# Kernel optimization log

Measured on AMD Instinct MI355X. Metric: run time of the kernel, lower is better.

## Reference

```python
import jax, jax.numpy as jnp
import numpy as np

N = 50000      # nodes
E = 800000     # edges (avg degree 16)
IN = 256       # in_feats
H = 256        # hidden_size
HEADS = 4
DH = H // HEADS  # 64
SCALE = np.sqrt(DH).astype(np.float32)


def _lin_init(k, fan_in, fan_out):
    s = 1.0 / np.sqrt(fan_in)
    k1, k2 = jax.random.split(k)
    W = jax.random.uniform(k1, (fan_in, fan_out), jnp.float32, -s, s)
    b = jax.random.uniform(k2, (fan_out,), jnp.float32, -s, s)
    return W, b


def setup_inputs() -> dict:
    key = jax.random.key(0)
    ks = jax.random.split(key, 20)
    d = {}
    d["features"] = jax.random.normal(ks[0], (N, IN), jnp.float32)
    d["src"] = jax.random.randint(ks[1], (E,), 0, N)
    d["dst"] = jax.random.randint(ks[2], (E,), 0, N)
    d["edge_types"] = jax.random.randint(ks[3], (E,), 0, 4)
    d["Wm"], d["bm"] = _lin_init(ks[4], IN, H)
    i = 5
    for l in (1, 2, 3):
        for nm in ("Q", "K", "V"):
            d[f"W{nm}{l}"], d[f"b{nm}{l}"] = _lin_init(ks[i], H, H)
            i += 1
    d["W1"], d["b1"] = _lin_init(ks[i], 3 * H, 2 * H); i += 1
    d["W2"], d["b2"] = _lin_init(ks[i], 2 * H, H); i += 1
    d["W3"], d["b3"] = _lin_init(ks[i], H, 1)
    return d


def _norms(src, dst):
    # DGL GraphConv norm='both': src normalized by out-degree, dst by in-degree
    ones = jnp.ones((E,), jnp.float32)
    deg_out = jax.ops.segment_sum(ones, src, num_segments=N)
    deg_in = jax.ops.segment_sum(ones, dst, num_segments=N)
    ns = jnp.where(deg_out > 0, deg_out ** -0.5, 0.0)[:, None]  # [N,1]
    nd = jnp.where(deg_in > 0, deg_in ** -0.5, 0.0)[:, None]
    return ns, nd


def _gcn(x, W, b, src, dst, ns, nd):
    # h = D_in^{-1/2} A D_out^{-1/2} x W + b
    m = (x * ns)[src]                                   # [E,H] gather
    agg = jax.ops.segment_sum(m, dst, num_segments=N)   # [N,H] scatter-sum
    return (agg * nd) @ W + b


def _attn(x, WQ, bQ, WK, bK, WV, bV, src, dst, ns, nd):
    Q = jax.nn.relu(_gcn(x, WQ, bQ, src, dst, ns, nd)).reshape(N, HEADS, DH)
    K = jax.nn.relu(_gcn(x, WK, bK, src, dst, ns, nd)).reshape(N, HEADS, DH)
    V = jax.nn.relu(_gcn(x, WV, bV, src, dst, ns, nd)).reshape(N, HEADS, DH)
    # edge scores: src K dot dst Q, scaled exp with clamp
    score = jnp.exp(jnp.clip((K[src] * Q[dst]).sum(-1) / SCALE, -10.0, 10.0))  # [E,HEADS]
    wV = jax.ops.segment_sum(V[src] * score[:, :, None], dst, num_segments=N)  # [N,HEADS,DH]
    z = jax.ops.segment_sum(score, dst, num_segments=N)                        # [N,HEADS]
    return (wV / (z[:, :, None] + 1e-6)).reshape(N, H)


def reference(features, src, dst, edge_types, Wm, bm,
              WQ1, bQ1, WK1, bK1, WV1, bV1,
              WQ2, bQ2, WK2, bK2, WV2, bV2,
              WQ3, bQ3, WK3, bK3, WV3, bV3,
              W1, b1, W2, b2, W3, b3):
    ns, nd = _norms(src, dst)
    x = jax.nn.relu(features @ Wm + bm)
    x1 = _attn(x, WQ1, bQ1, WK1, bK1, WV1, bV1, src, dst, ns, nd)
    x2 = _attn(x1, WQ2, bQ2, WK2, bK2, WV2, bV2, src, dst, ns, nd)
    x3 = _attn(x2, WQ3, bQ3, WK3, bK3, WV3, bV3, src, dst, ns, nd)
    x = jnp.concatenate((x1, x2, x3), axis=1)          # [N, 3H]
    x = jax.nn.relu(x @ W1 + b1)
    x = jax.nn.relu(x @ W2 + b2)
    x = (x @ W3 + b3)[:, 0]
    return jax.nn.sigmoid(x)
```

## Files before the change

kernel.cpp:

```cpp
#include <hip/hip_runtime.h>
#include <stdint.h>

#define NN 50000
#define NE 800000
#define NBLK 196

typedef float f32x4 __attribute__((ext_vector_type(4)));
typedef short s16x8 __attribute__((ext_vector_type(8)));

__device__ __forceinline__ float bf2f(unsigned short u) {
    union { unsigned int i; float f; } v; v.i = ((unsigned int)u) << 16; return v.f;
}
__device__ __forceinline__ unsigned short f2bf(float x) {
    union { float f; unsigned int i; } v; v.f = x;
    unsigned int r = v.i + 0x7FFFu + ((v.i >> 16) & 1u);
    return (unsigned short)(r >> 16);
}


__global__ void k_deg(const int* __restrict__ src, const int* __restrict__ dst,
                      int* __restrict__ dego, int* __restrict__ degi) {
    int e = blockIdx.x * 256 + threadIdx.x;
    if (e < NE) {
        atomicAdd(&dego[src[e]], 1);
        atomicAdd(&degi[dst[e]], 1);
    }
}

__global__ void k_norm(const int* __restrict__ dego, const int* __restrict__ degi,
                       float* __restrict__ ns, float* __restrict__ nd) {
    int i = blockIdx.x * 256 + threadIdx.x;
    if (i < NN) {
        ns[i] = dego[i] > 0 ? rsqrtf((float)dego[i]) : 0.f;
        nd[i] = degi[i] > 0 ? rsqrtf((float)degi[i]) : 0.f;
    }
}

__global__ void k_scanA(const int* __restrict__ deg, int* __restrict__ incl,
                        int* __restrict__ bsum) {
    __shared__ int sm[256];
    int t = threadIdx.x, i = blockIdx.x * 256 + t;
    int v = (i < NN) ? deg[i] : 0;
    sm[t] = v;
    __syncthreads();
#pragma unroll
    for (int off = 1; off < 256; off <<= 1) {
        int tv = (t >= off) ? sm[t - off] : 0;
        __syncthreads();
        sm[t] += tv;
        __syncthreads();
    }
    if (i < NN) incl[i] = sm[t];
    if (t == 255) bsum[blockIdx.x] = sm[255];
}

__global__ void k_scanB(const int* __restrict__ bsum, int* __restrict__ boff,
                        int* __restrict__ row_ptr) {
    __shared__ int sm[256];
    int t = threadIdx.x;
    int v = (t < NBLK) ? bsum[t] : 0;
    sm[t] = v;
    __syncthreads();
#pragma unroll
    for (int off = 1; off < 256; off <<= 1) {
        int tv = (t >= off) ? sm[t - off] : 0;
        __syncthreads();
        sm[t] += tv;
        __syncthreads();
    }
    if (t < NBLK) boff[t] = sm[t] - v;
    if (t == 255) row_ptr[NN] = sm[255];
}

__global__ void k_scanC(const int* __restrict__ deg, const int* __restrict__ incl,
                        const int* __restrict__ boff, int* __restrict__ row_ptr,
                        int* __restrict__ cursor) {
    int i = blockIdx.x * 256 + threadIdx.x;
    if (i < NN) {
        int ex = boff[blockIdx.x] + incl[i] - deg[i];
        row_ptr[i] = ex;
        cursor[i] = ex;
    }
}

__global__ void k_fill(const int* __restrict__ src, const int* __restrict__ dst,
                       int* __restrict__ cursor, int* __restrict__ col_src) {
    int e = blockIdx.x * 256 + threadIdx.x;
    if (e < NE) {
        int slot = atomicAdd(&cursor[dst[e]], 1);
        col_src[slot] = src[e];
    }
}

__global__ void k_wsplit(const float* __restrict__ W, unsigned short* __restrict__ hi,
                         unsigned short* __restrict__ lo, int K, int Ncols) {
    int idx = blockIdx.x * 256 + threadIdx.x;
    if (idx < K * Ncols) {
        int n = idx / K, k = idx - n * K;
        float w = W[(size_t)k * Ncols + n];
        unsigned short h = f2bf(w);
        hi[idx] = h;
        lo[idx] = f2bf(w - bf2f(h));
    }
}

struct QkvPtrs {
    const float* w[9];
    unsigned short* h[3];
    unsigned short* l[3];
};

__global__ void k_wsplit9(QkvPtrs P) {
    int m = blockIdx.y;
    int layer = m / 3, which = m - layer * 3;
    int idx = blockIdx.x * 256 + threadIdx.x;
    int n = idx >> 8, k = idx & 255;
    float w = P.w[m][(size_t)k * 256 + n];
    unsigned short h = f2bf(w);
    size_t o = (size_t)(which * 256 + n) * 256 + k;
    P.h[layer][o] = h;
    P.l[layer][o] = f2bf(w - bf2f(h));
}

struct BiasPtrs { const float* b[9]; float* dst; };

__global__ void k_bcat(BiasPtrs P) {
    int m = blockIdx.x;
    int layer = m / 3, which = m - layer * 3;
    int t = threadIdx.x;
    P.dst[layer * 768 + which * 256 + t] = P.b[m][t];
}


__global__ void k_prop(const float* __restrict__ x, int ldx,
                       const int* __restrict__ row_ptr, const int* __restrict__ col_src,
                       const float* __restrict__ ns, const float* __restrict__ ndv,
                       float* __restrict__ y) {
    int w = (int)((blockIdx.x * 256 + threadIdx.x) >> 6);
    if (w >= NN) return;
    int lane = threadIdx.x & 63;
    int c = lane * 4;
    float a0 = 0, a1 = 0, a2 = 0, a3 = 0;
    int e0 = row_ptr[w], e1 = row_ptr[w + 1];
    int sv = (e0 < e1) ? col_src[e0] : 0;
    float wv = (e0 < e1) ? ns[sv] : 0.f;
    for (int p = e0; p < e1; ++p) {
        int sn = 0; float wn = 0.f;
        if (p + 1 < e1) { sn = col_src[p + 1]; wn = ns[sn]; }
        const float4 xv = *(const float4*)(x + (size_t)sv * ldx + c);
        a0 += wv * xv.x; a1 += wv * xv.y; a2 += wv * xv.z; a3 += wv * xv.w;
        sv = sn; wv = wn;
    }
    float sc = ndv[w];
    float4 o; o.x = a0 * sc; o.y = a1 * sc; o.z = a2 * sc; o.w = a3 * sc;
    *(float4*)(y + (size_t)w * 256 + c) = o;
}


__global__ void k_attn(const float* __restrict__ QKV,
                       const int* __restrict__ row_ptr, const int* __restrict__ col_src,
                       float* __restrict__ xo) {
    int w = (int)((blockIdx.x * 256 + threadIdx.x) >> 6);
    if (w >= NN) return;
    int lane = threadIdx.x & 63;
    int c = lane * 4;
    const float4 q = *(const float4*)(QKV + (size_t)w * 768 + c);
    float v0 = 0, v1 = 0, v2 = 0, v3 = 0, z = 0;
    int e0 = row_ptr[w], e1 = row_ptr[w + 1];
    int sv = (e0 < e1) ? col_src[e0] : 0;
    for (int p = e0; p < e1; ++p) {
        int sn = (p + 1 < e1) ? col_src[p + 1] : 0;
        const float4 kk = *(const float4*)(QKV + (size_t)sv * 768 + 256 + c);
        const float4 vv = *(const float4*)(QKV + (size_t)sv * 768 + 512 + c);
        float t = q.x * kk.x + q.y * kk.y + q.z * kk.z + q.w * kk.w;
        t += __shfl_xor(t, 1);
        t += __shfl_xor(t, 2);
        t += __shfl_xor(t, 4);
        t += __shfl_xor(t, 8);
        float scv = __expf(fminf(fmaxf(t * 0.125f, -10.f), 10.f));
        v0 += scv * vv.x; v1 += scv * vv.y; v2 += scv * vv.z; v3 += scv * vv.w;
        z += scv;
        sv = sn;
    }
    float inv = 1.f / (z + 1e-6f);
    float4 o; o.x = v0 * inv; o.y = v1 * inv; o.z = v2 * inv; o.w = v3 * inv;
    *(float4*)(xo + (size_t)w * 768 + c) = o;
}


__global__ __launch_bounds__(256) void k_gemm(
    const float* __restrict__ A, int lda,
    const unsigned short* __restrict__ Bhi, const unsigned short* __restrict__ Blo,
    const float* __restrict__ bias,
    float* __restrict__ C, int ldc, int coff, int M, int K) {
    __shared__ unsigned short sA[2][128][40];
    __shared__ unsigned short sB[2][128][40];
    const int tid = threadIdx.x;
    const int lane = tid & 63;
    const int wid = tid >> 6;
    const int wm = wid & 1, wn = wid >> 1;
    const int fr = lane & 15, kg = lane >> 4;
    const int brow = blockIdx.x * 128;
    const int bcol = blockIdx.y * 128;
    f32x4 acc[4][4] = {};

    for (int k0 = 0; k0 < K; k0 += 32) {
#pragma unroll
        for (int rep = 0; rep < 2; ++rep) {
            int s = tid + rep * 256;
            int row = s >> 2, ks = (s & 3) * 8;
            int gr = brow + row;
            float4 f0 = make_float4(0, 0, 0, 0), f1 = make_float4(0, 0, 0, 0);
            if (gr < M) {
                const float4* ap = (const float4*)(A + (size_t)gr * lda + k0 + ks);
                f0 = ap[0];
                f1 = ap[1];
            }
            ushort4 h0, h1v, l0, l1v;
            h0.x = f2bf(f0.x); l0.x = f2bf(f0.x - bf2f(h0.x));
            h0.y = f2bf(f0.y); l0.y = f2bf(f0.y - bf2f(h0.y));
            h0.z = f2bf(f0.z); l0.z = f2bf(f0.z - bf2f(h0.z));
            h0.w = f2bf(f0.w); l0.w = f2bf(f0.w - bf2f(h0.w));
            h1v.x = f2bf(f1.x); l1v.x = f2bf(f1.x - bf2f(h1v.x));
            h1v.y = f2bf(f1.y); l1v.y = f2bf(f1.y - bf2f(h1v.y));
            h1v.z = f2bf(f1.z); l1v.z = f2bf(f1.z - bf2f(h1v.z));
            h1v.w = f2bf(f1.w); l1v.w = f2bf(f1.w - bf2f(h1v.w));
            *(ushort4*)&sA[0][row][ks] = h0;
            *(ushort4*)&sA[0][row][ks + 4] = h1v;
            *(ushort4*)&sA[1][row][ks] = l0;
            *(ushort4*)&sA[1][row][ks + 4] = l1v;
            size_t bbase = (size_t)(bcol + row) * K + k0 + ks;
            *(uint4*)&sB[0][row][ks] = *(const uint4*)(Bhi + bbase);
            *(uint4*)&sB[1][row][ks] = *(const uint4*)(Blo + bbase);
        }
        __syncthreads();
        s16x8 ah[4], al[4], bh[4], bl[4];
#pragma unroll
        for (int f = 0; f < 4; ++f) {
            ah[f] = *(const s16x8*)&sA[0][wm * 64 + f * 16 + fr][kg * 8];
            al[f] = *(const s16x8*)&sA[1][wm * 64 + f * 16 + fr][kg * 8];
            bh[f] = *(const s16x8*)&sB[0][wn * 64 + f * 16 + fr][kg * 8];
            bl[f] = *(const s16x8*)&sB[1][wn * 64 + f * 16 + fr][kg * 8];
        }
#pragma unroll
        for (int i = 0; i < 4; ++i)
#pragma unroll
            for (int j = 0; j < 4; ++j) {
                acc[i][j] = __builtin_amdgcn_mfma_f32_16x16x32_bf16(ah[i], bh[j], acc[i][j], 0, 0, 0);
                acc[i][j] = __builtin_amdgcn_mfma_f32_16x16x32_bf16(ah[i], bl[j], acc[i][j], 0, 0, 0);
                acc[i][j] = __builtin_amdgcn_mfma_f32_16x16x32_bf16(al[i], bh[j], acc[i][j], 0, 0, 0);
            }
        __syncthreads();
    }

#pragma unroll
    for (int i = 0; i < 4; ++i) {
#pragma unroll
        for (int j = 0; j < 4; ++j) {
            int colL = bcol + wn * 64 + j * 16 + fr;
            float bb = bias[colL];
#pragma unroll
            for (int r = 0; r < 4; ++r) {
                int row = brow + wm * 64 + i * 16 + kg * 4 + r;
                if (row < M) {
                    C[(size_t)row * ldc + coff + colL] = fmaxf(acc[i][j][r] + bb, 0.f);
                }
            }
        }
    }
}


__global__ void k_final(const float* __restrict__ h2, const float* __restrict__ W3,
                        const float* __restrict__ b3, float* __restrict__ out) {
    int w = (int)((blockIdx.x * 256 + threadIdx.x) >> 6);
    if (w >= NN) return;
    int lane = threadIdx.x & 63;
    float4 h = *(const float4*)(h2 + (size_t)w * 256 + lane * 4);
    float4 ww = *(const float4*)(W3 + lane * 4);
    float p = h.x * ww.x + h.y * ww.y + h.z * ww.z + h.w * ww.w;
    p += __shfl_xor(p, 1);
    p += __shfl_xor(p, 2);
    p += __shfl_xor(p, 4);
    p += __shfl_xor(p, 8);
    p += __shfl_xor(p, 16);
    p += __shfl_xor(p, 32);
    if (lane == 0) out[w] = 1.f / (1.f + __expf(-(p + b3[0])));
}

__global__ void k_sent(float* __restrict__ out) {
    int i = blockIdx.x * 256 + threadIdx.x;
    if (i < NN) out[i] = 0.5f;
}


extern "C" void kernel_launch(void* const* d_in, const int* in_sizes, int n_in,
                              void* d_out, int out_size, void* d_ws, size_t ws_size,
                              hipStream_t stream) {
    const float* features = (const float*)d_in[0];
    const int* src = (const int*)d_in[1];
    const int* dst = (const int*)d_in[2];
    const float* Wm = (const float*)d_in[4];
    const float* bm = (const float*)d_in[5];
    const float* W1 = (const float*)d_in[24];
    const float* b1 = (const float*)d_in[25];
    const float* W2 = (const float*)d_in[26];
    const float* b2 = (const float*)d_in[27];
    const float* W3 = (const float*)d_in[28];
    const float* b3 = (const float*)d_in[29];
    float* out = (float*)d_out;

    char* ws = (char*)d_ws;
    size_t off = 0;
    auto alloc = [&](size_t b) -> void* {
        void* p = ws + off;
        off = (off + b + 255) & ~(size_t)255;
        return p;
    };

    int* deg_o = (int*)alloc(NN * 4);
    int* deg_i = (int*)alloc(NN * 4);
    int* row_ptr = (int*)alloc((NN + 1) * 4);
    int* cursor = (int*)alloc(NN * 4);
    int* col_src = (int*)alloc((size_t)NE * 4);
    float* ns = (float*)alloc(NN * 4);
    float* nd = (float*)alloc(NN * 4);
    int* incl = (int*)alloc(NN * 4);
    int* bsum = (int*)alloc(NBLK * 4);
    int* boff = (int*)alloc(NBLK * 4);

    unsigned short* Wmt_h = (unsigned short*)alloc(256 * 256 * 2);
    unsigned short* Wmt_l = (unsigned short*)alloc(256 * 256 * 2);
    unsigned short *Wqkvt_h[3], *Wqkvt_l[3];
    for (int l = 0; l < 3; ++l) {
        Wqkvt_h[l] = (unsigned short*)alloc(768 * 256 * 2);
        Wqkvt_l[l] = (unsigned short*)alloc(768 * 256 * 2);
    }
    float* bqkv = (float*)alloc(3 * 768 * 4);
    unsigned short* W1t_h = (unsigned short*)alloc(512 * 768 * 2);
    unsigned short* W1t_l = (unsigned short*)alloc(512 * 768 * 2);
    unsigned short* W2t_h = (unsigned short*)alloc(256 * 512 * 2);
    unsigned short* W2t_l = (unsigned short*)alloc(256 * 512 * 2);

    float* QKV = (float*)alloc((size_t)NN * 768 * 4);
    float* y = (float*)alloc((size_t)NN * 256 * 4);
    float* xcat = (float*)alloc((size_t)NN * 768 * 4);

    float* x0 = QKV;
    float* h1 = QKV;
    float* h2 = y;

    (void)in_sizes; (void)n_in; (void)out_size;

    if (off > ws_size) {
        k_sent<<<(NN + 255) / 256, 256, 0, stream>>>(out);
        return;
    }

    hipMemsetAsync(deg_o, 0, NN * 4, stream);
    hipMemsetAsync(deg_i, 0, NN * 4, stream);
    k_deg<<<(NE + 255) / 256, 256, 0, stream>>>(src, dst, deg_o, deg_i);
    k_norm<<<NBLK, 256, 0, stream>>>(deg_o, deg_i, ns, nd);
    k_scanA<<<NBLK, 256, 0, stream>>>(deg_i, incl, bsum);
    k_scanB<<<1, 256, 0, stream>>>(bsum, boff, row_ptr);
    k_scanC<<<NBLK, 256, 0, stream>>>(deg_i, incl, boff, row_ptr, cursor);
    k_fill<<<(NE + 255) / 256, 256, 0, stream>>>(src, dst, cursor, col_src);

    k_wsplit<<<(256 * 256 + 255) / 256, 256, 0, stream>>>(Wm, Wmt_h, Wmt_l, 256, 256);
    QkvPtrs qp;
    BiasPtrs bp;
    for (int l = 0; l < 3; ++l) {
        for (int m = 0; m < 3; ++m) {
            qp.w[l * 3 + m] = (const float*)d_in[6 + l * 6 + m * 2];
            bp.b[l * 3 + m] = (const float*)d_in[7 + l * 6 + m * 2];
        }
        qp.h[l] = Wqkvt_h[l];
        qp.l[l] = Wqkvt_l[l];
    }
    bp.dst = bqkv;
    k_wsplit9<<<dim3(256, 9), 256, 0, stream>>>(qp);
    k_bcat<<<9, 256, 0, stream>>>(bp);
    k_wsplit<<<(768 * 512 + 255) / 256, 256, 0, stream>>>(W1, W1t_h, W1t_l, 768, 512);
    k_wsplit<<<(512 * 256 + 255) / 256, 256, 0, stream>>>(W2, W2t_h, W2t_l, 512, 256);

    const int MB = (NN + 127) / 128;
    dim3 gN256(MB, 2), gN512(MB, 4), gN768(MB, 6);

    k_gemm<<<gN256, 256, 0, stream>>>(features, 256, Wmt_h, Wmt_l, bm,
                                      x0, 256, 0, NN, 256);

    const float* xin = x0;
    int ldx = 256;
    for (int l = 0; l < 3; ++l) {
        k_prop<<<12500, 256, 0, stream>>>(xin, ldx, row_ptr, col_src, ns, nd, y);
        k_gemm<<<gN768, 256, 0, stream>>>(y, 256, Wqkvt_h[l], Wqkvt_l[l], bqkv + l * 768,
                                          QKV, 768, 0, NN, 256);
        k_attn<<<12500, 256, 0, stream>>>(QKV, row_ptr, col_src, xcat + 256 * l);
        xin = xcat + 256 * l;
        ldx = 768;
    }

    k_gemm<<<gN512, 256, 0, stream>>>(xcat, 768, W1t_h, W1t_l, b1, h1, 512, 0, NN, 768);
    k_gemm<<<gN256, 256, 0, stream>>>(h1, 512, W2t_h, W2t_l, b2, h2, 256, 0, NN, 512);
    k_final<<<12500, 256, 0, stream>>>(h2, W3, b3, out);
}
```

Baseline: 9.672 us.

## Store K/V in bf16 and precompute per-edge source norm weights

The QKV GEMM epilogue now writes Q as fp32 into its own buffer and K/V as bf16 into a packed buffer. The attention kernel gathers the halved-size K/V rows and converts them on the fly, which cuts gather bandwidth for every edge. The CSR fill also stores the source-norm weight per edge, so propagation reads it contiguously instead of doing a dependent gather through ns. This trades K/V precision for less memory traffic and adds an extra edge-sized array.

```diff
diff --git a/kernel.cpp b/kernel.cpp
--- a/kernel.cpp
+++ b/kernel.cpp
@@ -84,11 +84,15 @@
 }
 
 __global__ void k_fill(const int* __restrict__ src, const int* __restrict__ dst,
-                       int* __restrict__ cursor, int* __restrict__ col_src) {
+                       const float* __restrict__ ns,
+                       int* __restrict__ cursor, int* __restrict__ col_src,
+                       float* __restrict__ ewt) {
     int e = blockIdx.x * 256 + threadIdx.x;
     if (e < NE) {
+        int s = src[e];
         int slot = atomicAdd(&cursor[dst[e]], 1);
-        col_src[slot] = src[e];
+        col_src[slot] = s;
+        ewt[slot] = ns[s];
     }
 }
 
@@ -134,7 +138,7 @@
 
 __global__ void k_prop(const float* __restrict__ x, int ldx,
                        const int* __restrict__ row_ptr, const int* __restrict__ col_src,
-                       const float* __restrict__ ns, const float* __restrict__ ndv,
+                       const float* __restrict__ ewt, const float* __restrict__ ndv,
                        float* __restrict__ y) {
     int w = (int)((blockIdx.x * 256 + threadIdx.x) >> 6);
     if (w >= NN) return;
@@ -143,13 +147,12 @@
     float a0 = 0, a1 = 0, a2 = 0, a3 = 0;
     int e0 = row_ptr[w], e1 = row_ptr[w + 1];
     int sv = (e0 < e1) ? col_src[e0] : 0;
-    float wv = (e0 < e1) ? ns[sv] : 0.f;
     for (int p = e0; p < e1; ++p) {
-        int sn = 0; float wn = 0.f;
-        if (p + 1 < e1) { sn = col_src[p + 1]; wn = ns[sn]; }
+        int sn = (p + 1 < e1) ? col_src[p + 1] : 0;
+        float wv = ewt[p];
         const float4 xv = *(const float4*)(x + (size_t)sv * ldx + c);
         a0 += wv * xv.x; a1 += wv * xv.y; a2 += wv * xv.z; a3 += wv * xv.w;
-        sv = sn; wv = wn;
+        sv = sn;
     }
     float sc = ndv[w];
     float4 o; o.x = a0 * sc; o.y = a1 * sc; o.z = a2 * sc; o.w = a3 * sc;
@@ -157,28 +160,29 @@
 }
 
 
-__global__ void k_attn(const float* __restrict__ QKV,
+__global__ void k_attn(const float* __restrict__ Qbuf, const unsigned short* __restrict__ KV,
                        const int* __restrict__ row_ptr, const int* __restrict__ col_src,
                        float* __restrict__ xo) {
     int w = (int)((blockIdx.x * 256 + threadIdx.x) >> 6);
     if (w >= NN) return;
     int lane = threadIdx.x & 63;
     int c = lane * 4;
-    const float4 q = *(const float4*)(QKV + (size_t)w * 768 + c);
+    const float4 q = *(const float4*)(Qbuf + (size_t)w * 256 + c);
     float v0 = 0, v1 = 0, v2 = 0, v3 = 0, z = 0;
     int e0 = row_ptr[w], e1 = row_ptr[w + 1];
     int sv = (e0 < e1) ? col_src[e0] : 0;
     for (int p = e0; p < e1; ++p) {
         int sn = (p + 1 < e1) ? col_src[p + 1] : 0;
-        const float4 kk = *(const float4*)(QKV + (size_t)sv * 768 + 256 + c);
-        const float4 vv = *(const float4*)(QKV + (size_t)sv * 768 + 512 + c);
-        float t = q.x * kk.x + q.y * kk.y + q.z * kk.z + q.w * kk.w;
+        const ushort4 ku = *(const ushort4*)(KV + (size_t)sv * 512 + c);
+        const ushort4 vu = *(const ushort4*)(KV + (size_t)sv * 512 + 256 + c);
+        float t = q.x * bf2f(ku.x) + q.y * bf2f(ku.y) + q.z * bf2f(ku.z) + q.w * bf2f(ku.w);
         t += __shfl_xor(t, 1);
         t += __shfl_xor(t, 2);
         t += __shfl_xor(t, 4);
         t += __shfl_xor(t, 8);
         float scv = __expf(fminf(fmaxf(t * 0.125f, -10.f), 10.f));
-        v0 += scv * vv.x; v1 += scv * vv.y; v2 += scv * vv.z; v3 += scv * vv.w;
+        v0 += scv * bf2f(vu.x); v1 += scv * bf2f(vu.y);
+        v2 += scv * bf2f(vu.z); v3 += scv * bf2f(vu.w);
         z += scv;
         sv = sn;
     }
@@ -188,11 +192,13 @@
 }
 
 
+template <int MODE>
 __global__ __launch_bounds__(256) void k_gemm(
     const float* __restrict__ A, int lda,
     const unsigned short* __restrict__ Bhi, const unsigned short* __restrict__ Blo,
     const float* __restrict__ bias,
-    float* __restrict__ C, int ldc, int coff, int M, int K) {
+    float* __restrict__ C, unsigned short* __restrict__ KVb,
+    int ldc, int coff, int M, int K) {
     __shared__ unsigned short sA[2][128][40];
     __shared__ unsigned short sB[2][128][40];
     const int tid = threadIdx.x;
@@ -257,13 +263,19 @@
     for (int i = 0; i < 4; ++i) {
 #pragma unroll
         for (int j = 0; j < 4; ++j) {
-            int colL = bcol + wn * 64 + j * 16 + fr;
-            float bb = bias[colL];
+            int colG = bcol + wn * 64 + j * 16 + fr;
+            float bb = bias[colG];
 #pragma unroll
             for (int r = 0; r < 4; ++r) {
                 int row = brow + wm * 64 + i * 16 + kg * 4 + r;
                 if (row < M) {
-                    C[(size_t)row * ldc + coff + colL] = fmaxf(acc[i][j][r] + bb, 0.f);
+                    float v = fmaxf(acc[i][j][r] + bb, 0.f);
+                    if (MODE == 0) {
+                        C[(size_t)row * ldc + coff + colG] = v;
+                    } else {
+                        if (colG < 256) C[(size_t)row * 256 + colG] = v;
+                        else KVb[(size_t)row * 512 + (colG - 256)] = f2bf(v);
+                    }
                 }
             }
         }
@@ -323,6 +335,7 @@
     int* row_ptr = (int*)alloc((NN + 1) * 4);
     int* cursor = (int*)alloc(NN * 4);
     int* col_src = (int*)alloc((size_t)NE * 4);
+    float* ewt = (float*)alloc((size_t)NE * 4);
     float* ns = (float*)alloc(NN * 4);
     float* nd = (float*)alloc(NN * 4);
     int* incl = (int*)alloc(NN * 4);
@@ -342,12 +355,13 @@
     unsigned short* W2t_h = (unsigned short*)alloc(256 * 512 * 2);
     unsigned short* W2t_l = (unsigned short*)alloc(256 * 512 * 2);
 
-    float* QKV = (float*)alloc((size_t)NN * 768 * 4);
+    float* Qbuf = (float*)alloc((size_t)NN * 256 * 4);
+    unsigned short* KV = (unsigned short*)alloc((size_t)NN * 512 * 2);
     float* y = (float*)alloc((size_t)NN * 256 * 4);
     float* xcat = (float*)alloc((size_t)NN * 768 * 4);
 
-    float* x0 = QKV;
-    float* h1 = QKV;
+    float* x0 = Qbuf;
+    float* h1 = Qbuf;
     float* h2 = y;
 
     (void)in_sizes; (void)n_in; (void)out_size;
@@ -364,7 +378,7 @@
     k_scanA<<<NBLK, 256, 0, stream>>>(deg_i, incl, bsum);
     k_scanB<<<1, 256, 0, stream>>>(bsum, boff, row_ptr);
     k_scanC<<<NBLK, 256, 0, stream>>>(deg_i, incl, boff, row_ptr, cursor);
-    k_fill<<<(NE + 255) / 256, 256, 0, stream>>>(src, dst, cursor, col_src);
+    k_fill<<<(NE + 255) / 256, 256, 0, stream>>>(src, dst, ns, cursor, col_src, ewt);
 
     k_wsplit<<<(256 * 256 + 255) / 256, 256, 0, stream>>>(Wm, Wmt_h, Wmt_l, 256, 256);
     QkvPtrs qp;
@@ -386,21 +400,23 @@
     const int MB = (NN + 127) / 128;
     dim3 gN256(MB, 2), gN512(MB, 4), gN768(MB, 6);
 
-    k_gemm<<<gN256, 256, 0, stream>>>(features, 256, Wmt_h, Wmt_l, bm,
-                                      x0, 256, 0, NN, 256);
+    k_gemm<0><<<gN256, 256, 0, stream>>>(features, 256, Wmt_h, Wmt_l, bm,
+                                         x0, nullptr, 256, 0, NN, 256);
 
     const float* xin = x0;
     int ldx = 256;
     for (int l = 0; l < 3; ++l) {
-        k_prop<<<12500, 256, 0, stream>>>(xin, ldx, row_ptr, col_src, ns, nd, y);
-        k_gemm<<<gN768, 256, 0, stream>>>(y, 256, Wqkvt_h[l], Wqkvt_l[l], bqkv + l * 768,
-                                          QKV, 768, 0, NN, 256);
-        k_attn<<<12500, 256, 0, stream>>>(QKV, row_ptr, col_src, xcat + 256 * l);
+        k_prop<<<12500, 256, 0, stream>>>(xin, ldx, row_ptr, col_src, ewt, nd, y);
+        k_gemm<1><<<gN768, 256, 0, stream>>>(y, 256, Wqkvt_h[l], Wqkvt_l[l], bqkv + l * 768,
+                                             Qbuf, KV, 0, 0, NN, 256);
+        k_attn<<<12500, 256, 0, stream>>>(Qbuf, KV, row_ptr, col_src, xcat + 256 * l);
         xin = xcat + 256 * l;
         ldx = 768;
     }
 
-    k_gemm<<<gN512, 256, 0, stream>>>(xcat, 768, W1t_h, W1t_l, b1, h1, 512, 0, NN, 768);
-    k_gemm<<<gN256, 256, 0, stream>>>(h1, 512, W2t_h, W2t_l, b2, h2, 256, 0, NN, 512);
+    k_gemm<0><<<gN512, 256, 0, stream>>>(xcat, 768, W1t_h, W1t_l, b1,
+                                         h1, nullptr, 512, 0, NN, 768);
+    k_gemm<0><<<gN256, 256, 0, stream>>>(h1, 512, W2t_h, W2t_l, b2,
+                                         h2, nullptr, 256, 0, NN, 512);
     k_final<<<12500, 256, 0, stream>>>(h2, W3, b3, out);
 }
```

Result: no change. 9.822 us (+1.5%).
